# Performance work log

Hardware: AMD Instinct MI355X
Metric: run time of the kernel (lower is better)

The kernel has to match this reference:

```python
import jax, jax.numpy as jnp
import numpy as np

N, M, KLEN, D_MODEL, H = 256, 256, 128, 256, 8
DK = D_MODEL // H


def _linear_params(key, out_dim, in_dim):
    # torch nn.Linear default init: U(-1/sqrt(in), 1/sqrt(in))
    kw, kb = jax.random.split(key)
    bound = 1.0 / np.sqrt(in_dim)
    W = jax.random.uniform(kw, (out_dim, in_dim), jnp.float32, -bound, bound)
    b = jax.random.uniform(kb, (out_dim,), jnp.float32, -bound, bound)
    return W, b


def setup_inputs() -> dict:
    key = jax.random.key(0)
    ks = jax.random.split(key, 7)
    query = jax.random.normal(ks[0], (N, D_MODEL), jnp.float32)
    key_t = jax.random.normal(ks[1], (M, KLEN, D_MODEL), jnp.float32)
    value = jax.random.normal(ks[2], (M, KLEN, D_MODEL), jnp.float32)
    Wq, bq = _linear_params(ks[3], D_MODEL, D_MODEL)
    Wk, bk = _linear_params(ks[4], D_MODEL, D_MODEL)
    Wv, bv = _linear_params(ks[5], D_MODEL, D_MODEL)
    Wo, bo = _linear_params(ks[6], D_MODEL, D_MODEL)
    return {"query": query, "key": key_t, "value": value,
            "Wq": Wq, "bq": bq, "Wk": Wk, "bk": bk,
            "Wv": Wv, "bv": bv, "Wo": Wo, "bo": bo}


def reference(query, key, value, Wq, bq, Wk, bk, Wv, bv, Wo, bo):
    n = query.shape[0]
    m = key.shape[0]
    # projections (torch Linear: x @ W.T + b)
    q = (query @ Wq.T + bq).reshape(n, H, DK)                      # [n,h,d]
    k = (key @ Wk.T + bk).reshape(m, -1, H, DK).transpose(0, 2, 1, 3)   # [m,h,k,d]
    v = (value @ Wv.T + bv).reshape(m, -1, H, DK).transpose(0, 2, 1, 3)  # [m,h,k,d]
    # cross-batch attention scores: [n,m,h,k]
    scores = jnp.einsum('nhd,mhkd->nmhk', q, k) / np.sqrt(DK).astype(np.float32)
    p_attn = jax.nn.softmax(scores, axis=-1)
    # context: [n,m,h,d] -> [n,m,d_model]
    ctx = jnp.einsum('nmhk,mhkd->nmhd', p_attn, v).reshape(n, m, H * DK)
    return ctx @ Wo.T + bo
```

## Files before the change

kernel.cpp:

```cpp
#include <hip/hip_runtime.h>


typedef unsigned short u16;
typedef unsigned int u32;
typedef __attribute__((ext_vector_type(8))) _Float16 half8;
typedef __attribute__((ext_vector_type(4))) _Float16 half4;
typedef __attribute__((ext_vector_type(4))) float f32x4;
typedef __attribute__((ext_vector_type(4))) unsigned short us4;
typedef __attribute__((ext_vector_type(2))) unsigned int u32x2;

__device__ __forceinline__ u16 f2h(float v) {
  _Float16 h = (_Float16)v;
  return __builtin_bit_cast(u16, h);
}
__device__ __forceinline__ u32 pk2(float lo, float hi) {
  return (u32)f2h(lo) | ((u32)f2h(hi) << 16);
}
__device__ __forceinline__ u32 pkrtz(float lo, float hi) {
  return __builtin_bit_cast(u32, __builtin_amdgcn_cvt_pkrtz(lo, hi));
}
__device__ __forceinline__ f32x4 mf16(half8 a, half8 b, f32x4 c) {
  return __builtin_amdgcn_mfma_f32_16x16x32_f16(a, b, c, 0, 0, 0);
}
__device__ __forceinline__ f32x4 mf16k16(half4 a, half4 b, f32x4 c) {
  return __builtin_amdgcn_mfma_f32_16x16x16f16(a, b, c, 0, 0, 0);
}
__device__ __forceinline__ void gload_lds16(const void* g, void* l) {
  __builtin_amdgcn_global_load_lds((const __attribute__((address_space(1))) u32*)g,
                                   (__attribute__((address_space(3))) u32*)l, 16, 0, 0);
}

__global__ __launch_bounds__(256) void wcvt_kernel(const float* __restrict__ Wq,
                                                   const float* __restrict__ Wk,
                                                   const float* __restrict__ Wv,
                                                   const float* __restrict__ Wo,
                                                   u16* __restrict__ wfq, u16* __restrict__ wfk,
                                                   u16* __restrict__ wfv, u16* __restrict__ wof) {
  int t = blockIdx.x * 256 + threadIdx.x;
  int widx = t >> 13, tl = t & 8191;
  int ln = tl & 63, kk = (tl >> 6) & 7, jt = tl >> 9;
  const float* src = widx == 0 ? Wq : widx == 1 ? Wk : widx == 2 ? Wv : Wo;
  u16* dst = widx == 0 ? wfq : widx == 1 ? wfk : widx == 2 ? wfv : wof;
  int j = jt * 16 + (ln & 15);
  int k0 = kk * 32 + (ln >> 4) * 8;
  float4 g0 = *(const float4*)(src + j * 256 + k0);
  float4 g1 = *(const float4*)(src + j * 256 + k0 + 4);
  us4 h0 = { f2h(g0.x), f2h(g0.y), f2h(g0.z), f2h(g0.w) };
  us4 h1 = { f2h(g1.x), f2h(g1.y), f2h(g1.z), f2h(g1.w) };
  int idx8 = (widx == 3) ? ((kk * 16 + jt) * 64 + ln)
                         : ((jt * 8 + kk) * 64 + ln);
  *(us4*)(dst + idx8 * 8) = h0;
  *(us4*)(dst + idx8 * 8 + 4) = h1;
}

__global__ __launch_bounds__(256, 4) void proj_all_kernel(const float* __restrict__ query,
                                                          const float* __restrict__ key,
                                                          const float* __restrict__ value,
                                                          const u16* __restrict__ wfq,
                                                          const u16* __restrict__ wfk,
                                                          const u16* __restrict__ wfv,
                                                          const float* __restrict__ bq,
                                                          const float* __restrict__ bk,
                                                          const float* __restrict__ bv,
                                                          u16* __restrict__ qp,
                                                          u16* __restrict__ kfrag,
                                                          u16* __restrict__ vt3) {
  __shared__ __align__(16) u16 xa[64 * 256];
  int bid = blockIdx.x;
  int mode, logical;
  const float* X; const u16* wf; const float* bias; u16* out;
  if (bid < 2048) {
    mode = 1; X = key; wf = wfk; bias = bk; out = kfrag;
    logical = (bid & 7) * 256 + (bid >> 3);
  } else if (bid < 4096) {
    int b = bid - 2048;
    mode = 2; X = value; wf = wfv; bias = bv; out = vt3;
    logical = (b & 7) * 256 + (b >> 3);
  } else {
    mode = 0; X = query; wf = wfq; bias = bq; out = qp;
    logical = bid - 4096;
  }
  int rb = logical >> 2, cb = logical & 3;
  int tid = threadIdx.x;
  char* xb = (char*)xa;
#pragma unroll
  for (int i = 0; i < 16; ++i) {
    int idx = tid + i * 256;
    int row = idx >> 6, c4 = idx & 63;
    int so = (row * 512 + c4 * 8) ^ ((row & 7) << 4);
    float4 gx = *(const float4*)(X + (rb * 64 + row) * 256 + c4 * 4);
    us4 hx = { f2h(gx.x), f2h(gx.y), f2h(gx.z), f2h(gx.w) };
    *(us4*)(xb + so) = hx;
  }
  __syncthreads();

  int lane = tid & 63, w = tid >> 6;
  int lr = lane & 15, lq = lane >> 4;

  if (mode == 2) {
    half8 a[8];
#pragma unroll
    for (int kk = 0; kk < 8; ++kk)
      a[kk] = *(const half8*)(xb + (((w * 16 + lr) * 512 + kk * 64 + lq * 16) ^ ((lr & 7) << 4)));
#pragma unroll
    for (int ct = 0; ct < 4; ++ct) {
      int jtile = cb * 4 + ct;
      f32x4 acc = {0.f, 0.f, 0.f, 0.f};
#pragma unroll
      for (int kk = 0; kk < 8; ++kk) {
        half8 b = *(const half8*)(wf + ((jtile * 8 + kk) * 64 + lane) * 8);
        acc = mf16(a[kk], b, acc);
      }
      int j = jtile * 16 + lr;
      float bj = bias[j];
      int h = j >> 5, d = j & 31;
      int gr0 = rb * 64 + w * 16 + lq * 4;
      int mm = gr0 >> 7, kl0 = gr0 & 127;
      int base = (((mm * 8 + h) * 2 + (d >> 4)) * 8 + (kl0 >> 4)) * 256
               + (((kl0 >> 2) & 3) * 16 + (d & 15)) * 4;
      us4 st = { f2h(acc[0] + bj), f2h(acc[1] + bj), f2h(acc[2] + bj), f2h(acc[3] + bj) };
      *(us4*)(out + base) = st;
    }
  } else {
    int jtile = cb * 4 + w;
    half8 a[8];
#pragma unroll
    for (int kk = 0; kk < 8; ++kk)
      a[kk] = *(const half8*)(wf + ((jtile * 8 + kk) * 64 + lane) * 8);
    int j0 = jtile * 16 + lq * 4;
    float4 bv4 = *(const float4*)(bias + j0);
    int h = j0 >> 5, d0 = j0 & 31;
#pragma unroll
    for (int ct = 0; ct < 4; ++ct) {
      f32x4 acc = {0.f, 0.f, 0.f, 0.f};
#pragma unroll
      for (int kk = 0; kk < 8; ++kk) {
        half8 b = *(const half8*)(xb + (((ct * 16 + lr) * 512 + kk * 64 + lq * 16) ^ ((lr & 7) << 4)));
        acc = mf16(a[kk], b, acc);
      }
      int gr = rb * 64 + ct * 16 + lr;
      us4 st = { f2h(acc[0] + bv4.x), f2h(acc[1] + bv4.y), f2h(acc[2] + bv4.z), f2h(acc[3] + bv4.w) };
      if (mode == 0) {
        *(us4*)(out + gr * 256 + j0) = st;
      } else {
        int mm = gr >> 7, kl = gr & 127;
        int idx = (mm * 8 + h) * 4096 + (kl >> 4) * 512
                + ((d0 >> 3) * 16 + (kl & 15)) * 8 + (d0 & 7);
        *(us4*)(out + idx) = st;
      }
    }
  }
}

__global__ __launch_bounds__(512, 4) void fused_attn_kernel(const u16* __restrict__ qp,
                                                            const u16* __restrict__ kp,
                                                            const u16* __restrict__ vt3,
                                                            const u16* __restrict__ wof,
                                                            const float* __restrict__ bo,
                                                            float* __restrict__ out) {
  __shared__ __align__(16) u16 kbuf[2][4096];
  __shared__ __align__(16) u16 vbuf[2][4096];
  __shared__ __align__(16) u16 cbuf[2][4096];

  const int bid = blockIdx.x;
  const int xcd = bid & 7, idx = bid >> 3;
  const int m = xcd * 32 + (idx >> 1);
  const int nh = idx & 1;
  const int tid = threadIdx.x;
  const int w = tid >> 6, lane = tid & 63;
  const int lr = lane & 15, lq = lane >> 4;
  const int n0 = nh * 128 + w * 16;
  const float SCL2E = 0.25506980508f;

  const char* kg = (const char*)(kp + m * 8 * 4096);
  const char* vg = (const char*)(vt3 + m * 8 * 4096);

  gload_lds16(kg + w * 1024 + lane * 16, (char*)(&kbuf[0][0]) + w * 1024);
  gload_lds16(vg + w * 1024 + lane * 16, (char*)(&vbuf[0][0]) + w * 1024);
  __syncthreads();

  f32x4 accO[2][8];
#pragma unroll
  for (int jt = 0; jt < 2; ++jt)
#pragma unroll
    for (int nb = 0; nb < 8; ++nb) accO[jt][nb] = f32x4{0.f, 0.f, 0.f, 0.f};

  for (int h = 0; h < 8; ++h) {
    const int cur = h & 1;
    char* kb = (char*)(&kbuf[cur][0]);
    char* vb = (char*)(&vbuf[cur][0]);
    char* cb = (char*)(&cbuf[cur][0]);
    if (h < 7) {
      gload_lds16(kg + (h + 1) * 8192 + w * 1024 + lane * 16, (char*)(&kbuf[cur ^ 1][0]) + w * 1024);
      gload_lds16(vg + (h + 1) * 8192 + w * 1024 + lane * 16, (char*)(&vbuf[cur ^ 1][0]) + w * 1024);
    }
    half8 qa = *(const half8*)(qp + (n0 + lr) * 256 + h * 32 + lq * 8);
    f32x4 s[8];
    __builtin_amdgcn_s_setprio(1);
#pragma unroll
    for (int kt = 0; kt < 8; ++kt) {
      half8 ka = *(const half8*)(kb + kt * 1024 + lane * 16);
      f32x4 z = {0.f, 0.f, 0.f, 0.f};
      s[kt] = mf16(ka, qa, z);
    }
    __builtin_amdgcn_s_setprio(0);
    float sA = 0.f, sB = 0.f;
    half4 pb[8];
#pragma unroll
    for (int kt = 0; kt < 8; ++kt) {
      float p0 = __builtin_amdgcn_exp2f(s[kt][0] * SCL2E);
      float p1 = __builtin_amdgcn_exp2f(s[kt][1] * SCL2E);
      float p2 = __builtin_amdgcn_exp2f(s[kt][2] * SCL2E);
      float p3 = __builtin_amdgcn_exp2f(s[kt][3] * SCL2E);
      sA += p0 + p1; sB += p2 + p3;
      u32x2 pw = { pkrtz(p0, p1), pkrtz(p2, p3) };
      pb[kt] = __builtin_bit_cast(half4, pw);
    }
    float sum = sA + sB;
    sum += __shfl_xor(sum, 16);
    sum += __shfl_xor(sum, 32);
    float inv = 1.0f / sum;
    f32x4 a0 = {0.f, 0.f, 0.f, 0.f}, a1 = {0.f, 0.f, 0.f, 0.f};
    __builtin_amdgcn_s_setprio(1);
#pragma unroll
    for (int kt = 0; kt < 8; ++kt) {
      half4 v0 = *(const half4*)(vb + kt * 512 + lane * 8);
      a0 = mf16k16(v0, pb[kt], a0);
      half4 v1 = *(const half4*)(vb + 4096 + kt * 512 + lane * 8);
      a1 = mf16k16(v1, pb[kt], a1);
    }
    __builtin_amdgcn_s_setprio(0);
    half8 wv0 = *(const half8*)(wof + ((h * 16 + w * 2 + 0) * 64 + lane) * 8);
    half8 wv1 = *(const half8*)(wof + ((h * 16 + w * 2 + 1) * 64 + lane) * 8);
    u32x2 c0 = { pk2(a0[0] * inv, a0[1] * inv), pk2(a0[2] * inv, a0[3] * inv) };
    u32x2 c1 = { pk2(a1[0] * inv, a1[1] * inv), pk2(a1[2] * inv, a1[3] * inv) };
    const int cwo = w * 1024 + ((lq >> 1) * 16 + lr) * 16 + (lq & 1) * 8;
    *(u32x2*)(cb + cwo) = c0;
    *(u32x2*)(cb + cwo + 512) = c1;
    __syncthreads();
    __builtin_amdgcn_s_setprio(1);
#pragma unroll
    for (int nb = 0; nb < 8; ++nb) {
      half8 cf = *(const half8*)(cb + nb * 1024 + lane * 16);
      accO[0][nb] = mf16(wv0, cf, accO[0][nb]);
      accO[1][nb] = mf16(wv1, cf, accO[1][nb]);
    }
    __builtin_amdgcn_s_setprio(0);
  }
#pragma unroll
  for (int jt = 0; jt < 2; ++jt) {
    const int j0 = w * 32 + jt * 16 + lq * 4;
    float4 bv = *(const float4*)(bo + j0);
#pragma unroll
    for (int nb = 0; nb < 8; ++nb) {
      const int n = nh * 128 + nb * 16 + lr;
      float4 r;
      r.x = accO[jt][nb][0] + bv.x;
      r.y = accO[jt][nb][1] + bv.y;
      r.z = accO[jt][nb][2] + bv.z;
      r.w = accO[jt][nb][3] + bv.w;
      *(float4*)(out + (n * 256 + m) * 256 + j0) = r;
    }
  }
}

extern "C" void kernel_launch(void* const* d_in, const int* in_sizes, int n_in,
                              void* d_out, int out_size, void* d_ws, size_t ws_size,
                              hipStream_t stream) {
  (void)in_sizes; (void)n_in; (void)out_size; (void)ws_size;
  const float* query = (const float*)d_in[0];
  const float* key   = (const float*)d_in[1];
  const float* value = (const float*)d_in[2];
  const float* Wq = (const float*)d_in[3];
  const float* bq = (const float*)d_in[4];
  const float* Wk = (const float*)d_in[5];
  const float* bk = (const float*)d_in[6];
  const float* Wv = (const float*)d_in[7];
  const float* bv = (const float*)d_in[8];
  const float* Wo = (const float*)d_in[9];
  const float* bo = (const float*)d_in[10];
  float* out = (float*)d_out;

  u16* ws = (u16*)d_ws;
  u16* kfrag = ws;
  u16* vt3   = kfrag + 8388608;
  u16* qp    = vt3 + 8388608;
  u16* wof   = qp + 65536;
  u16* wfq   = wof + 65536;
  u16* wfk   = wfq + 65536;
  u16* wfv   = wfk + 65536;

  wcvt_kernel<<<128, 256, 0, stream>>>(Wq, Wk, Wv, Wo, wfq, wfk, wfv, wof);
  proj_all_kernel<<<4112, 256, 0, stream>>>(query, key, value, wfq, wfk, wfv,
                                            bq, bk, bv, qp, kfrag, vt3);
  fused_attn_kernel<<<512, 512, 0, stream>>>(qp, kfrag, vt3, wof, bo, out);
}
```

Measured before the change: 69.95 us.

## Split fused attention into 4 warps per block with 1024 blocks

Each block of the fused attention kernel now covers 64 query rows instead of 128, using 4 waves of 256 threads, and the grid doubles to 1024 blocks. Each wave computes 64 output columns, so it loads four Wo fragments instead of two, and the K/V staging loads are spread across fewer threads. A second barrier is added at the end of each head iteration. The aim is more blocks and better occupancy, but every K/V tile for a given m is now loaded by twice as many blocks, which raises global/L2 traffic.

```diff
diff --git a/kernel.cpp b/kernel.cpp
--- a/kernel.cpp
+++ b/kernel.cpp
@@ -152,7 +152,7 @@
   }
 }
 
-__global__ __launch_bounds__(512, 4) void fused_attn_kernel(const u16* __restrict__ qp,
+__global__ __launch_bounds__(256, 4) void fused_attn_kernel(const u16* __restrict__ qp,
                                                             const u16* __restrict__ kp,
                                                             const u16* __restrict__ vt3,
                                                             const u16* __restrict__ wof,
@@ -160,30 +160,32 @@
                                                             float* __restrict__ out) {
   __shared__ __align__(16) u16 kbuf[2][4096];
   __shared__ __align__(16) u16 vbuf[2][4096];
-  __shared__ __align__(16) u16 cbuf[2][4096];
+  __shared__ __align__(16) u16 cbuf[2][2048];
 
   const int bid = blockIdx.x;
   const int xcd = bid & 7, idx = bid >> 3;
-  const int m = xcd * 32 + (idx >> 1);
-  const int nh = idx & 1;
+  const int m = xcd * 32 + (idx >> 2);
+  const int nq = idx & 3;
   const int tid = threadIdx.x;
   const int w = tid >> 6, lane = tid & 63;
   const int lr = lane & 15, lq = lane >> 4;
-  const int n0 = nh * 128 + w * 16;
+  const int n0 = nq * 64 + w * 16;
   const float SCL2E = 0.25506980508f;
 
   const char* kg = (const char*)(kp + m * 8 * 4096);
   const char* vg = (const char*)(vt3 + m * 8 * 4096);
 
-  gload_lds16(kg + w * 1024 + lane * 16, (char*)(&kbuf[0][0]) + w * 1024);
-  gload_lds16(vg + w * 1024 + lane * 16, (char*)(&vbuf[0][0]) + w * 1024);
+  gload_lds16(kg + tid * 16, (char*)(&kbuf[0][0]) + tid * 16);
+  gload_lds16(kg + 4096 + tid * 16, (char*)(&kbuf[0][0]) + 4096 + tid * 16);
+  gload_lds16(vg + tid * 16, (char*)(&vbuf[0][0]) + tid * 16);
+  gload_lds16(vg + 4096 + tid * 16, (char*)(&vbuf[0][0]) + 4096 + tid * 16);
   __syncthreads();
 
-  f32x4 accO[2][8];
-#pragma unroll
-  for (int jt = 0; jt < 2; ++jt)
-#pragma unroll
-    for (int nb = 0; nb < 8; ++nb) accO[jt][nb] = f32x4{0.f, 0.f, 0.f, 0.f};
+  f32x4 accO[4][4];
+#pragma unroll
+  for (int jj = 0; jj < 4; ++jj)
+#pragma unroll
+    for (int nb = 0; nb < 4; ++nb) accO[jj][nb] = f32x4{0.f, 0.f, 0.f, 0.f};
 
   for (int h = 0; h < 8; ++h) {
     const int cur = h & 1;
@@ -191,8 +193,12 @@
     char* vb = (char*)(&vbuf[cur][0]);
     char* cb = (char*)(&cbuf[cur][0]);
     if (h < 7) {
-      gload_lds16(kg + (h + 1) * 8192 + w * 1024 + lane * 16, (char*)(&kbuf[cur ^ 1][0]) + w * 1024);
-      gload_lds16(vg + (h + 1) * 8192 + w * 1024 + lane * 16, (char*)(&vbuf[cur ^ 1][0]) + w * 1024);
+      char* kn = (char*)(&kbuf[cur ^ 1][0]);
+      char* vn = (char*)(&vbuf[cur ^ 1][0]);
+      gload_lds16(kg + (h + 1) * 8192 + tid * 16, kn + tid * 16);
+      gload_lds16(kg + (h + 1) * 8192 + 4096 + tid * 16, kn + 4096 + tid * 16);
+      gload_lds16(vg + (h + 1) * 8192 + tid * 16, vn + tid * 16);
+      gload_lds16(vg + (h + 1) * 8192 + 4096 + tid * 16, vn + 4096 + tid * 16);
     }
     half8 qa = *(const half8*)(qp + (n0 + lr) * 256 + h * 32 + lq * 8);
     f32x4 s[8];
@@ -230,8 +236,10 @@
       a1 = mf16k16(v1, pb[kt], a1);
     }
     __builtin_amdgcn_s_setprio(0);
-    half8 wv0 = *(const half8*)(wof + ((h * 16 + w * 2 + 0) * 64 + lane) * 8);
-    half8 wv1 = *(const half8*)(wof + ((h * 16 + w * 2 + 1) * 64 + lane) * 8);
+    half8 wv0 = *(const half8*)(wof + ((h * 16 + w * 4 + 0) * 64 + lane) * 8);
+    half8 wv1 = *(const half8*)(wof + ((h * 16 + w * 4 + 1) * 64 + lane) * 8);
+    half8 wv2 = *(const half8*)(wof + ((h * 16 + w * 4 + 2) * 64 + lane) * 8);
+    half8 wv3 = *(const half8*)(wof + ((h * 16 + w * 4 + 3) * 64 + lane) * 8);
     u32x2 c0 = { pk2(a0[0] * inv, a0[1] * inv), pk2(a0[2] * inv, a0[3] * inv) };
     u32x2 c1 = { pk2(a1[0] * inv, a1[1] * inv), pk2(a1[2] * inv, a1[3] * inv) };
     const int cwo = w * 1024 + ((lq >> 1) * 16 + lr) * 16 + (lq & 1) * 8;
@@ -240,25 +248,28 @@
     __syncthreads();
     __builtin_amdgcn_s_setprio(1);
 #pragma unroll
-    for (int nb = 0; nb < 8; ++nb) {
+    for (int nb = 0; nb < 4; ++nb) {
       half8 cf = *(const half8*)(cb + nb * 1024 + lane * 16);
       accO[0][nb] = mf16(wv0, cf, accO[0][nb]);
       accO[1][nb] = mf16(wv1, cf, accO[1][nb]);
+      accO[2][nb] = mf16(wv2, cf, accO[2][nb]);
+      accO[3][nb] = mf16(wv3, cf, accO[3][nb]);
     }
     __builtin_amdgcn_s_setprio(0);
-  }
-#pragma unroll
-  for (int jt = 0; jt < 2; ++jt) {
-    const int j0 = w * 32 + jt * 16 + lq * 4;
+    __syncthreads();
+  }
+#pragma unroll
+  for (int jj = 0; jj < 4; ++jj) {
+    const int j0 = (w * 4 + jj) * 16 + lq * 4;
     float4 bv = *(const float4*)(bo + j0);
 #pragma unroll
-    for (int nb = 0; nb < 8; ++nb) {
-      const int n = nh * 128 + nb * 16 + lr;
+    for (int nb = 0; nb < 4; ++nb) {
+      const int n = nq * 64 + nb * 16 + lr;
       float4 r;
-      r.x = accO[jt][nb][0] + bv.x;
-      r.y = accO[jt][nb][1] + bv.y;
-      r.z = accO[jt][nb][2] + bv.z;
-      r.w = accO[jt][nb][3] + bv.w;
+      r.x = accO[jj][nb][0] + bv.x;
+      r.y = accO[jj][nb][1] + bv.y;
+      r.z = accO[jj][nb][2] + bv.z;
+      r.w = accO[jj][nb][3] + bv.w;
       *(float4*)(out + (n * 256 + m) * 256 + j0) = r;
     }
   }
@@ -293,5 +304,5 @@
   wcvt_kernel<<<128, 256, 0, stream>>>(Wq, Wk, Wv, Wo, wfq, wfk, wfv, wof);
   proj_all_kernel<<<4112, 256, 0, stream>>>(query, key, value, wfq, wfk, wfv,
                                             bq, bk, bv, qp, kfrag, vt3);
-  fused_attn_kernel<<<512, 512, 0, stream>>>(qp, kfrag, vt3, wof, bo, out);
-}
+  fused_attn_kernel<<<1024, 256, 0, stream>>>(qp, kfrag, vt3, wof, bo, out);
+}
```

Result: slower. 71.80 us (+2.6%).

## Split input fp16 conversion into separate pre-swizzled pass before projection

Applied to the files above, without the earlier changes.

Adds a kernel that converts query, key and value to fp16 in MFMA fragment order, writing the key/value copies into the output buffer as scratch. The projection kernel then loads fragments directly from global memory, with no LDS staging or __syncthreads, and can run at higher occupancy. In exchange, each input now takes an extra global round trip (fp32 read, fp16 write, fp16 read), and each X tile is re-read by four column blocks instead of being shared through LDS.

```diff
diff --git a/kernel.cpp b/kernel.cpp
--- a/kernel.cpp
+++ b/kernel.cpp
@@ -53,55 +53,65 @@
   *(us4*)(dst + idx8 * 8 + 4) = h1;
 }
 
-__global__ __launch_bounds__(256, 4) void proj_all_kernel(const float* __restrict__ query,
-                                                          const float* __restrict__ key,
-                                                          const float* __restrict__ value,
-                                                          const u16* __restrict__ wfq,
-                                                          const u16* __restrict__ wfk,
-                                                          const u16* __restrict__ wfv,
-                                                          const float* __restrict__ bq,
-                                                          const float* __restrict__ bk,
-                                                          const float* __restrict__ bv,
-                                                          u16* __restrict__ qp,
-                                                          u16* __restrict__ kfrag,
-                                                          u16* __restrict__ vt3) {
-  __shared__ __align__(16) u16 xa[64 * 256];
+__global__ __launch_bounds__(256) void xcvt_kernel(const float* __restrict__ query,
+                                                   const float* __restrict__ key,
+                                                   const float* __restrict__ value,
+                                                   u16* __restrict__ xq,
+                                                   u16* __restrict__ xk,
+                                                   u16* __restrict__ xv) {
+  int bid = blockIdx.x;
+  const float* src; u16* dst; int e;
+  if (bid < 4096)      { src = key;   dst = xk; e = bid * 256 + threadIdx.x; }
+  else if (bid < 8192) { src = value; dst = xv; e = (bid - 4096) * 256 + threadIdx.x; }
+  else                 { src = query; dst = xq; e = (bid - 8192) * 256 + threadIdx.x; }
+  int ln = e & 63, kk = (e >> 6) & 7, rt = e >> 9;
+  int row = rt * 16 + (ln & 15);
+  int c0 = kk * 32 + (ln >> 4) * 8;
+  float4 g0 = *(const float4*)(src + row * 256 + c0);
+  float4 g1 = *(const float4*)(src + row * 256 + c0 + 4);
+  us4 h0 = { f2h(g0.x), f2h(g0.y), f2h(g0.z), f2h(g0.w) };
+  us4 h1 = { f2h(g1.x), f2h(g1.y), f2h(g1.z), f2h(g1.w) };
+  *(us4*)(dst + e * 8) = h0;
+  *(us4*)(dst + e * 8 + 4) = h1;
+}
+
+__global__ __launch_bounds__(256, 6) void proj_lite_kernel(const u16* __restrict__ xq,
+                                                           const u16* __restrict__ xk,
+                                                           const u16* __restrict__ xv,
+                                                           const u16* __restrict__ wfq,
+                                                           const u16* __restrict__ wfk,
+                                                           const u16* __restrict__ wfv,
+                                                           const float* __restrict__ bq,
+                                                           const float* __restrict__ bk,
+                                                           const float* __restrict__ bv,
+                                                           u16* __restrict__ qp,
+                                                           u16* __restrict__ kfrag,
+                                                           u16* __restrict__ vt3) {
   int bid = blockIdx.x;
   int mode, logical;
-  const float* X; const u16* wf; const float* bias; u16* out;
+  const u16* xf; const u16* wf; const float* bias; u16* out;
   if (bid < 2048) {
-    mode = 1; X = key; wf = wfk; bias = bk; out = kfrag;
+    mode = 1; xf = xk; wf = wfk; bias = bk; out = kfrag;
     logical = (bid & 7) * 256 + (bid >> 3);
   } else if (bid < 4096) {
     int b = bid - 2048;
-    mode = 2; X = value; wf = wfv; bias = bv; out = vt3;
+    mode = 2; xf = xv; wf = wfv; bias = bv; out = vt3;
     logical = (b & 7) * 256 + (b >> 3);
   } else {
-    mode = 0; X = query; wf = wfq; bias = bq; out = qp;
+    mode = 0; xf = xq; wf = wfq; bias = bq; out = qp;
     logical = bid - 4096;
   }
   int rb = logical >> 2, cb = logical & 3;
   int tid = threadIdx.x;
-  char* xb = (char*)xa;
-#pragma unroll
-  for (int i = 0; i < 16; ++i) {
-    int idx = tid + i * 256;
-    int row = idx >> 6, c4 = idx & 63;
-    int so = (row * 512 + c4 * 8) ^ ((row & 7) << 4);
-    float4 gx = *(const float4*)(X + (rb * 64 + row) * 256 + c4 * 4);
-    us4 hx = { f2h(gx.x), f2h(gx.y), f2h(gx.z), f2h(gx.w) };
-    *(us4*)(xb + so) = hx;
-  }
-  __syncthreads();
-
   int lane = tid & 63, w = tid >> 6;
   int lr = lane & 15, lq = lane >> 4;
 
   if (mode == 2) {
+    int rt = rb * 4 + w;
     half8 a[8];
 #pragma unroll
     for (int kk = 0; kk < 8; ++kk)
-      a[kk] = *(const half8*)(xb + (((w * 16 + lr) * 512 + kk * 64 + lq * 16) ^ ((lr & 7) << 4)));
+      a[kk] = *(const half8*)(xf + ((rt * 8 + kk) * 64 + lane) * 8);
 #pragma unroll
     for (int ct = 0; ct < 4; ++ct) {
       int jtile = cb * 4 + ct;
@@ -114,7 +124,7 @@
       int j = jtile * 16 + lr;
       float bj = bias[j];
       int h = j >> 5, d = j & 31;
-      int gr0 = rb * 64 + w * 16 + lq * 4;
+      int gr0 = rt * 16 + lq * 4;
       int mm = gr0 >> 7, kl0 = gr0 & 127;
       int base = (((mm * 8 + h) * 2 + (d >> 4)) * 8 + (kl0 >> 4)) * 256
                + (((kl0 >> 2) & 3) * 16 + (d & 15)) * 4;
@@ -132,13 +142,14 @@
     int h = j0 >> 5, d0 = j0 & 31;
 #pragma unroll
     for (int ct = 0; ct < 4; ++ct) {
+      int rt = rb * 4 + ct;
       f32x4 acc = {0.f, 0.f, 0.f, 0.f};
 #pragma unroll
       for (int kk = 0; kk < 8; ++kk) {
-        half8 b = *(const half8*)(xb + (((ct * 16 + lr) * 512 + kk * 64 + lq * 16) ^ ((lr & 7) << 4)));
+        half8 b = *(const half8*)(xf + ((rt * 8 + kk) * 64 + lane) * 8);
         acc = mf16(a[kk], b, acc);
       }
-      int gr = rb * 64 + ct * 16 + lr;
+      int gr = rt * 16 + lr;
       us4 st = { f2h(acc[0] + bv4.x), f2h(acc[1] + bv4.y), f2h(acc[2] + bv4.z), f2h(acc[3] + bv4.w) };
       if (mode == 0) {
         *(us4*)(out + gr * 256 + j0) = st;
@@ -289,9 +300,13 @@
   u16* wfq   = wof + 65536;
   u16* wfk   = wfq + 65536;
   u16* wfv   = wfk + 65536;
+  u16* xq    = wfv + 65536;
+  u16* xk = (u16*)d_out;
+  u16* xv = xk + 8388608;
 
   wcvt_kernel<<<128, 256, 0, stream>>>(Wq, Wk, Wv, Wo, wfq, wfk, wfv, wof);
-  proj_all_kernel<<<4112, 256, 0, stream>>>(query, key, value, wfq, wfk, wfv,
-                                            bq, bk, bv, qp, kfrag, vt3);
+  xcvt_kernel<<<8224, 256, 0, stream>>>(query, key, value, xq, xk, xv);
+  proj_lite_kernel<<<4112, 256, 0, stream>>>(xq, xk, xv, wfq, wfk, wfv,
+                                             bq, bk, bv, qp, kfrag, vt3);
   fused_attn_kernel<<<512, 512, 0, stream>>>(qp, kfrag, vt3, wof, bo, out);
 }
```

Result: slower. 86.23 us (+23.3%).
